# Kernel tuning notes

Measured on AMD Instinct MI355X. Metric: run time of the kernel, lower is better.

## Reference

```python
import jax, jax.numpy as jnp
import numpy as np

N_E = 1024      # nconcepts (codebook size)
E_DIM = 64      # cdim (codebook vector dim)
BETA = 0.25
LEGACY = True


def setup_inputs() -> dict:
    key = jax.random.key(0)
    k1, k2, k3 = jax.random.split(key, 3)
    z_ = jax.random.normal(k1, (32, 256, 32, 32), jnp.float32)
    # 1x1 conv dis_modulator: 256 -> 64 channels (stored as [out, in])
    conv_w = jax.random.normal(k2, (64, 256), jnp.float32) / np.sqrt(256.0)
    conv_b = jnp.zeros((64,), jnp.float32)
    # embedding.weight.data.uniform_(-1/n_e, 1/n_e)
    emb = jax.random.uniform(k3, (N_E, E_DIM), jnp.float32, -1.0 / N_E, 1.0 / N_E)
    return {"z_": z_, "conv_w": conv_w, "conv_b": conv_b, "emb": emb}


def _forward(z_, conv_w, conv_b, emb):
    sg = jax.lax.stop_gradient
    # dis_modulator: 1x1 conv == per-pixel linear map  (B,Cin,H,W)->(B,Cout,H,W)
    z = jnp.einsum('bchw,oc->bohw', z_, conv_w) + conv_b[None, :, None, None]
    B = z.shape[0]
    # torch .view(-1, e_dim): row-major flatten of (B,C,H,W) into chunks of e_dim
    zf = z.reshape(-1, E_DIM)  # [B*C*H*W/e_dim, e_dim]

    # contrastive term: mean pairwise cosine similarity of codebook rows
    d1 = emb @ emb.T                                  # [n_e, n_e]
    norms = jnp.linalg.norm(emb, axis=1)              # [n_e]
    cosine = d1 / (norms[:, None] * norms[None, :])
    contrastive = jnp.mean(cosine)

    # squared L2 distances: ||z||^2 + ||e||^2 - 2 z.e
    d = (jnp.sum(zf * zf, axis=1, keepdims=True)
         + jnp.sum(emb * emb, axis=1)[None, :]
         - 2.0 * (zf @ emb.T))                        # [N, n_e]
    idx = jnp.argmin(d, axis=1)                       # [N]
    z_q = emb[idx].reshape(z.shape)

    if LEGACY:
        loss = jnp.mean((sg(z_q) - z) ** 2) + BETA * jnp.mean((z_q - sg(z)) ** 2)
    else:
        loss = BETA * jnp.mean((sg(z_q) - z) ** 2) + jnp.mean((z_q - sg(z)) ** 2)
    # hessian_penalty(G, z_, G_z=z): G is an affine 1x1 conv, so the central
    # second difference G(z+x) - 2G(z) + G(z-x) is identically zero -> penalty = 0.
    loss = loss + contrastive

    # straight-through estimator
    z_q_st = z + sg(z_q - z)

    # replicate source exactly: flat zeros(B*n_e) scattered at codebook indices
    sampled = jnp.zeros((B * N_E,), z.dtype).at[idx].set(1.0).reshape(B, N_E)
    min_idx = idx.reshape(B, -1)
    return z_q_st, loss, sampled, min_idx


def reference(z_, conv_w, conv_b, emb):
    z_q, loss, sampled, min_idx = _forward(z_, conv_w, conv_b, emb)
    return z_q, loss, sampled, min_idx
```

## Files before the change

### kernel.cpp

```cpp
#include <hip/hip_runtime.h>

#define BATCH   32
#define CIN     256
#define COUT    64
#define HW      1024
#define NE      1024
#define ED      64
#define NROW    32768
#define ZTOT    2097152

#define OFF_LOSS 2097152
#define OFF_SAMP 2097153
#define OFF_IDX  2129921

#define CXSTR 132
#define CWSTR 68
#define ZSTR  132
#define ESTR2 260

__global__ __launch_bounds__(256, 2) void k_pre(const float* __restrict__ x,
                                                const float* __restrict__ w,
                                                const float* __restrict__ bias,
                                                float* __restrict__ z,
                                                const float* __restrict__ emb,
                                                float* __restrict__ out_samp,
                                                float* __restrict__ enorm,
                                                float* __restrict__ cpart) {
    __shared__ float SH[64 * CXSTR + 64 * CWSTR];
    int bx = blockIdx.x;
    int t  = threadIdx.x;

    if (bx < 128) {
        out_samp[bx * 256 + t] = 0.0f;
        return;
    }
    if (bx < 144) {
        float* invl = SH;
        float* S    = SH + 64;
        int b2 = bx - 128;
        int i0 = b2 * 64;
        if (t < 64) {
            const float* e = emb + (size_t)(i0 + t) * ED;
            float r8[8];
            #pragma unroll
            for (int s = 0; s < 8; s++) { float xx = e[s]; r8[s] = xx * xx; }
            #pragma unroll
            for (int m = 1; m < 8; m++) {
                #pragma unroll
                for (int s = 0; s < 8; s++) { float xx = e[8 * m + s]; r8[s] += xx * xx; }
            }
            float en = ((r8[0] + r8[1]) + (r8[2] + r8[3])) + ((r8[4] + r8[5]) + (r8[6] + r8[7]));
            invl[t] = 1.0f / sqrtf(en);
        }
        __syncthreads();
        int d = t & 63, q = t >> 6;
        float s = 0.0f;
        #pragma unroll
        for (int m = 0; m < 16; m++) {
            int il = q + 4 * m;
            s = fmaf(emb[(size_t)(i0 + il) * ED + d], invl[il], s);
        }
        S[t] = s;
        __syncthreads();
        if (t < 64)
            cpart[b2 * 64 + t] = (S[t] + S[t + 64]) + (S[t + 128] + S[t + 192]);
        return;
    }
    if (bx < 148) {
        int j = (bx - 144) * 256 + t;
        const float* e = emb + (size_t)j * ED;
        float r8[8];
        #pragma unroll
        for (int s = 0; s < 8; s++) { float xx = e[s]; r8[s] = xx * xx; }
        #pragma unroll
        for (int m = 1; m < 8; m++) {
            #pragma unroll
            for (int s = 0; s < 8; s++) { float xx = e[8 * m + s]; r8[s] += xx * xx; }
        }
        enorm[j] = ((r8[0] + r8[1]) + (r8[2] + r8[3])) + ((r8[4] + r8[5]) + (r8[6] + r8[7]));
        return;
    }

    float* Xs = SH;
    float* Ws = SH + 64 * CXSTR;
    int cbx = bx - 148;
    int b   = cbx >> 3;
    int p0  = (cbx & 7) * 128;
    int pg  = t & 15;
    int og  = t >> 4;
    float acc[8][4];
    #pragma unroll
    for (int i = 0; i < 8; i++)
        #pragma unroll
        for (int j = 0; j < 4; j++) acc[i][j] = 0.0f;

    for (int c0 = 0; c0 < CIN; c0 += 64) {
        __syncthreads();
        {
            int u = t & 31, cc = t >> 5;
            #pragma unroll
            for (int m = 0; m < 8; m++) {
                int c = cc + 8 * m;
                float4 v = *(const float4*)&x[(size_t)(b * CIN + c0 + c) * HW + p0 + 4 * u];
                *(float4*)&Xs[c * CXSTR + 4 * u] = v;
            }
            int u2 = t & 15, o2 = t >> 4;
            #pragma unroll
            for (int m = 0; m < 4; m++) {
                int o = o2 + 16 * m;
                float4 v = *(const float4*)&w[o * CIN + c0 + 4 * u2];
                Ws[(4 * u2 + 0) * CWSTR + o] = v.x;
                Ws[(4 * u2 + 1) * CWSTR + o] = v.y;
                Ws[(4 * u2 + 2) * CWSTR + o] = v.z;
                Ws[(4 * u2 + 3) * CWSTR + o] = v.w;
            }
        }
        __syncthreads();
        #pragma unroll 4
        for (int k = 0; k < 64; k++) {
            float4 xa4 = *(const float4*)&Xs[k * CXSTR + 4 * pg];
            float4 xb4 = *(const float4*)&Xs[k * CXSTR + 64 + 4 * pg];
            float4 wv4 = *(const float4*)&Ws[k * CWSTR + 4 * og];
            float xa[8] = {xa4.x, xa4.y, xa4.z, xa4.w, xb4.x, xb4.y, xb4.z, xb4.w};
            float wb[4] = {wv4.x, wv4.y, wv4.z, wv4.w};
            #pragma unroll
            for (int i = 0; i < 8; i++)
                #pragma unroll
                for (int j = 0; j < 4; j++)
                    acc[i][j] = fmaf(xa[i], wb[j], acc[i][j]);
        }
    }
    #pragma unroll
    for (int j = 0; j < 4; j++) {
        int o = 4 * og + j;
        float bv = bias[o];
        float4 lo, hi;
        lo.x = acc[0][j] + bv; lo.y = acc[1][j] + bv;
        lo.z = acc[2][j] + bv; lo.w = acc[3][j] + bv;
        hi.x = acc[4][j] + bv; hi.y = acc[5][j] + bv;
        hi.z = acc[6][j] + bv; hi.w = acc[7][j] + bv;
        *(float4*)&z[(size_t)(b * COUT + o) * HW + p0 + 4 * pg]      = lo;
        *(float4*)&z[(size_t)(b * COUT + o) * HW + p0 + 64 + 4 * pg] = hi;
    }
}

__global__ __launch_bounds__(256, 1) void k_dist(const float* __restrict__ z,
                                                 const float* __restrict__ emb,
                                                 const float* __restrict__ enorm,
                                                 float* __restrict__ out_idx,
                                                 float* __restrict__ out_samp,
                                                 float* __restrict__ out_zq,
                                                 float* __restrict__ ssep) {
    __shared__ float zs[64 * ZSTR];
    __shared__ float es[64 * ESTR2];
    __shared__ float zn_s[128];
    __shared__ float en_s[256];
    __shared__ float warr[4];
    float* redd_s = es;
    int*   redj_s = (int*)(es + 2048);
    int*   bj_s   = (int*)(es + 4096);
    int t = threadIdx.x;
    int row0 = blockIdx.x * 128;
    int rg = t & 15;
    int cg = t >> 4;

    {
        int k = t & 63, wv = t >> 6;
        #pragma unroll
        for (int m = 0; m < 8; m++) {
            int v = wv + 4 * m;
            float4 val;
            val.x = z[(size_t)(row0 + 4 * v + 0) * ED + k];
            val.y = z[(size_t)(row0 + 4 * v + 1) * ED + k];
            val.z = z[(size_t)(row0 + 4 * v + 2) * ED + k];
            val.w = z[(size_t)(row0 + 4 * v + 3) * ED + k];
            *(float4*)&zs[k * ZSTR + 4 * v] = val;
        }
    }
    __syncthreads();
    if (t < 128) {
        float r8[8];
        #pragma unroll
        for (int s = 0; s < 8; s++) { float xx = zs[s * ZSTR + t]; r8[s] = xx * xx; }
        #pragma unroll
        for (int m = 1; m < 8; m++) {
            #pragma unroll
            for (int s = 0; s < 8; s++) { float xx = zs[(8 * m + s) * ZSTR + t]; r8[s] += xx * xx; }
        }
        zn_s[t] = ((r8[0] + r8[1]) + (r8[2] + r8[3])) + ((r8[4] + r8[5]) + (r8[6] + r8[7]));
    }

    float bestd[8];
    int   bestj[8];
    #pragma unroll
    for (int i = 0; i < 8; i++) { bestd[i] = __builtin_huge_valf(); bestj[i] = 0; }

    for (int ch = 0; ch < 4; ch++) {
        int c0 = ch * 256;
        __syncthreads();
        {
            int k = t & 63, wv = t >> 6;
            #pragma unroll
            for (int m = 0; m < 16; m++) {
                int v = wv + 4 * m;
                float4 val;
                val.x = emb[(size_t)(c0 + 4 * v + 0) * ED + k];
                val.y = emb[(size_t)(c0 + 4 * v + 1) * ED + k];
                val.z = emb[(size_t)(c0 + 4 * v + 2) * ED + k];
                val.w = emb[(size_t)(c0 + 4 * v + 3) * ED + k];
                *(float4*)&es[k * ESTR2 + 4 * v] = val;
            }
            if (t < 64) {
                float4 ev4 = *(const float4*)&enorm[c0 + 4 * t];
                *(float4*)&en_s[4 * t] = ev4;
            }
        }
        __syncthreads();

        float acc[8][16];
        #pragma unroll
        for (int i = 0; i < 8; i++)
            #pragma unroll
            for (int j = 0; j < 16; j++) acc[i][j] = 0.0f;

        #pragma unroll 2
        for (int k = 0; k < 64; k++) {
            float4 za = *(const float4*)&zs[k * ZSTR + 4 * rg];
            float4 zb = *(const float4*)&zs[k * ZSTR + 64 + 4 * rg];
            float4 e0 = *(const float4*)&es[k * ESTR2 + 16 * cg];
            float4 e1 = *(const float4*)&es[k * ESTR2 + 16 * cg + 4];
            float4 e2 = *(const float4*)&es[k * ESTR2 + 16 * cg + 8];
            float4 e3 = *(const float4*)&es[k * ESTR2 + 16 * cg + 12];
            float xa[8]  = {za.x, za.y, za.z, za.w, zb.x, zb.y, zb.z, zb.w};
            float eb[16] = {e0.x, e0.y, e0.z, e0.w, e1.x, e1.y, e1.z, e1.w,
                            e2.x, e2.y, e2.z, e2.w, e3.x, e3.y, e3.z, e3.w};
            #pragma unroll
            for (int i = 0; i < 8; i++)
                #pragma unroll
                for (int j = 0; j < 16; j++)
                    acc[i][j] = fmaf(xa[i], eb[j], acc[i][j]);
        }

        #pragma unroll
        for (int i = 0; i < 8; i++) {
            int rl = (i < 4) ? (4 * rg + i) : (64 + 4 * rg + (i - 4));
            float zn = zn_s[rl];
            #pragma unroll
            for (int j = 0; j < 16; j++) {
                int cl = 16 * cg + j;
                float A = zn + en_s[cl];
                float D = A - 2.0f * acc[i][j];
                if (D < bestd[i]) { bestd[i] = D; bestj[i] = c0 + cl; }
            }
        }
    }

    __syncthreads();
    #pragma unroll
    for (int i = 0; i < 8; i++) {
        int rl = (i < 4) ? (4 * rg + i) : (64 + 4 * rg + (i - 4));
        redd_s[cg * 128 + rl] = bestd[i];
        redj_s[cg * 128 + rl] = bestj[i];
    }
    __syncthreads();
    if (t < 128) {
        float bd = __builtin_huge_valf();
        int   bj = 0x7fffffff;
        #pragma unroll
        for (int c = 0; c < 16; c++) {
            float dd = redd_s[c * 128 + t];
            int   jj = redj_s[c * 128 + t];
            if (dd < bd || (dd == bd && jj < bj)) { bd = dd; bj = jj; }
        }
        int rowg = row0 + t;
        bj_s[t]       = bj;
        out_idx[rowg] = (float)bj;
        atomicExch(&out_samp[bj], 1.0f);
    }
    __syncthreads();

    {
        int r  = t & 127;
        int kq = t >> 7;
        int bj = bj_s[r];
        const float* er = emb + (size_t)bj * ED + kq * 32;
        float sq = 0.0f;
        #pragma unroll
        for (int m = 0; m < 8; m++) {
            float4 ev = *(const float4*)&er[4 * m];
            int kk = kq * 32 + 4 * m;
            float zv0 = zs[(kk + 0) * ZSTR + r];
            float zv1 = zs[(kk + 1) * ZSTR + r];
            float zv2 = zs[(kk + 2) * ZSTR + r];
            float zv3 = zs[(kk + 3) * ZSTR + r];
            float d0 = ev.x - zv0, d1 = ev.y - zv1, d2 = ev.z - zv2, d3 = ev.w - zv3;
            float4 o4;
            o4.x = zv0 + d0; o4.y = zv1 + d1; o4.z = zv2 + d2; o4.w = zv3 + d3;
            *(float4*)&out_zq[(size_t)(row0 + r) * ED + kk] = o4;
            sq += d0 * d0; sq += d1 * d1; sq += d2 * d2; sq += d3 * d3;
        }
        #pragma unroll
        for (int off = 32; off > 0; off >>= 1) sq += __shfl_down(sq, off, 64);
        if ((t & 63) == 0) warr[t >> 6] = sq;
    }
    __syncthreads();
    if (t == 0)
        ssep[blockIdx.x] = (warr[0] + warr[1]) + (warr[2] + warr[3]);
}

__global__ __launch_bounds__(256) void k_final(const float* __restrict__ ssep,
                                               const float* __restrict__ cpart,
                                               float* __restrict__ out_loss) {
    __shared__ double SD[256];
    __shared__ float  CS;
    int t = threadIdx.x;
    SD[t] = (double)ssep[t];
    __syncthreads();
    #pragma unroll
    for (int off = 128; off > 0; off >>= 1) {
        if (t < off) SD[t] += SD[t + off];
        __syncthreads();
    }
    if (t < 64) {
        float v = 0.0f;
        #pragma unroll
        for (int m = 0; m < 16; m++) v += cpart[m * 64 + t];
        float sq = v * v;
        #pragma unroll
        for (int off = 32; off > 0; off >>= 1) sq += __shfl_down(sq, off, 64);
        if (t == 0) CS = sq / (1024.0f * 1024.0f);
    }
    __syncthreads();
    if (t == 0) {
        float m = (float)(SD[0] / (double)ZTOT);
        float loss = m + 0.25f * m;
        out_loss[0] = loss + CS;
    }
}

extern "C" void kernel_launch(void* const* d_in, const int* in_sizes, int n_in,
                              void* d_out, int out_size, void* d_ws, size_t ws_size,
                              hipStream_t stream) {
    (void)in_sizes; (void)n_in; (void)out_size; (void)ws_size;
    const float* z_     = (const float*)d_in[0];
    const float* conv_w = (const float*)d_in[1];
    const float* conv_b = (const float*)d_in[2];
    const float* emb    = (const float*)d_in[3];

    float* out      = (float*)d_out;
    float* out_zq   = out;
    float* out_loss = out + OFF_LOSS;
    float* out_samp = out + OFF_SAMP;
    float* out_idx  = out + OFF_IDX;

    char*  ws       = (char*)d_ws;
    float* wz       = (float*)ws;
    float* enorm    = (float*)(ws + 8388608);
    float* cpart    = (float*)(ws + 8396800);
    float* ssep     = (float*)(ws + 8400896);

    k_pre  <<<404, 256, 0, stream>>>(z_, conv_w, conv_b, wz, emb, out_samp, enorm, cpart);
    k_dist <<<256, 256, 0, stream>>>(wz, emb, enorm, out_idx, out_samp, out_zq, ssep);
    k_final<<<1,   256, 0, stream>>>(ssep, cpart, out_loss);
}
```

Baseline: 179.5 us.

## Shrink distance tile to raise occupancy and fold final reduction into last block

```diff
diff --git a/kernel.cpp b/kernel.cpp
--- a/kernel.cpp
+++ b/kernel.cpp
@@ -16,7 +16,7 @@
 #define CXSTR 132
 #define CWSTR 68
 #define ZSTR  132
-#define ESTR2 260
+#define ESTR  132
 
 __global__ __launch_bounds__(256, 2) void k_pre(const float* __restrict__ x,
                                                 const float* __restrict__ w,
@@ -25,12 +25,14 @@
                                                 const float* __restrict__ emb,
                                                 float* __restrict__ out_samp,
                                                 float* __restrict__ enorm,
-                                                float* __restrict__ cpart) {
+                                                float* __restrict__ cpart,
+                                                unsigned int* __restrict__ counter) {
     __shared__ float SH[64 * CXSTR + 64 * CWSTR];
     int bx = blockIdx.x;
     int t  = threadIdx.x;
 
     if (bx < 128) {
+        if (bx == 0 && t == 0) *counter = 0u;
         out_samp[bx * 256 + t] = 0.0f;
         return;
     }
@@ -144,18 +146,23 @@
     }
 }
 
-__global__ __launch_bounds__(256, 1) void k_dist(const float* __restrict__ z,
+__global__ __launch_bounds__(256, 2) void k_dist(const float* __restrict__ z,
                                                  const float* __restrict__ emb,
                                                  const float* __restrict__ enorm,
+                                                 const float* __restrict__ cpart,
                                                  float* __restrict__ out_idx,
                                                  float* __restrict__ out_samp,
                                                  float* __restrict__ out_zq,
-                                                 float* __restrict__ ssep) {
+                                                 float* __restrict__ ssep,
+                                                 float* __restrict__ out_loss,
+                                                 unsigned int* __restrict__ counter) {
     __shared__ float zs[64 * ZSTR];
-    __shared__ float es[64 * ESTR2];
+    __shared__ float es[64 * ESTR];
     __shared__ float zn_s[128];
-    __shared__ float en_s[256];
+    __shared__ float en_s[128];
     __shared__ float warr[4];
+    __shared__ int   lastflag;
+    __shared__ float CS;
     float* redd_s = es;
     int*   redj_s = (int*)(es + 2048);
     int*   bj_s   = (int*)(es + 4096);
@@ -195,49 +202,46 @@
     #pragma unroll
     for (int i = 0; i < 8; i++) { bestd[i] = __builtin_huge_valf(); bestj[i] = 0; }
 
-    for (int ch = 0; ch < 4; ch++) {
-        int c0 = ch * 256;
+    for (int ch = 0; ch < 8; ch++) {
+        int c0 = ch * 128;
         __syncthreads();
         {
             int k = t & 63, wv = t >> 6;
             #pragma unroll
-            for (int m = 0; m < 16; m++) {
+            for (int m = 0; m < 8; m++) {
                 int v = wv + 4 * m;
                 float4 val;
                 val.x = emb[(size_t)(c0 + 4 * v + 0) * ED + k];
                 val.y = emb[(size_t)(c0 + 4 * v + 1) * ED + k];
                 val.z = emb[(size_t)(c0 + 4 * v + 2) * ED + k];
                 val.w = emb[(size_t)(c0 + 4 * v + 3) * ED + k];
-                *(float4*)&es[k * ESTR2 + 4 * v] = val;
-            }
-            if (t < 64) {
+                *(float4*)&es[k * ESTR + 4 * v] = val;
+            }
+            if (t < 32) {
                 float4 ev4 = *(const float4*)&enorm[c0 + 4 * t];
                 *(float4*)&en_s[4 * t] = ev4;
             }
         }
         __syncthreads();
 
-        float acc[8][16];
+        float acc[8][8];
         #pragma unroll
         for (int i = 0; i < 8; i++)
             #pragma unroll
-            for (int j = 0; j < 16; j++) acc[i][j] = 0.0f;
-
-        #pragma unroll 2
+            for (int j = 0; j < 8; j++) acc[i][j] = 0.0f;
+
+        #pragma unroll 4
         for (int k = 0; k < 64; k++) {
             float4 za = *(const float4*)&zs[k * ZSTR + 4 * rg];
             float4 zb = *(const float4*)&zs[k * ZSTR + 64 + 4 * rg];
-            float4 e0 = *(const float4*)&es[k * ESTR2 + 16 * cg];
-            float4 e1 = *(const float4*)&es[k * ESTR2 + 16 * cg + 4];
-            float4 e2 = *(const float4*)&es[k * ESTR2 + 16 * cg + 8];
-            float4 e3 = *(const float4*)&es[k * ESTR2 + 16 * cg + 12];
-            float xa[8]  = {za.x, za.y, za.z, za.w, zb.x, zb.y, zb.z, zb.w};
-            float eb[16] = {e0.x, e0.y, e0.z, e0.w, e1.x, e1.y, e1.z, e1.w,
-                            e2.x, e2.y, e2.z, e2.w, e3.x, e3.y, e3.z, e3.w};
+            float4 e0 = *(const float4*)&es[k * ESTR + 8 * cg];
+            float4 e1 = *(const float4*)&es[k * ESTR + 8 * cg + 4];
+            float xa[8] = {za.x, za.y, za.z, za.w, zb.x, zb.y, zb.z, zb.w};
+            float eb[8] = {e0.x, e0.y, e0.z, e0.w, e1.x, e1.y, e1.z, e1.w};
             #pragma unroll
             for (int i = 0; i < 8; i++)
                 #pragma unroll
-                for (int j = 0; j < 16; j++)
+                for (int j = 0; j < 8; j++)
                     acc[i][j] = fmaf(xa[i], eb[j], acc[i][j]);
         }
 
@@ -246,8 +250,8 @@
             int rl = (i < 4) ? (4 * rg + i) : (64 + 4 * rg + (i - 4));
             float zn = zn_s[rl];
             #pragma unroll
-            for (int j = 0; j < 16; j++) {
-                int cl = 16 * cg + j;
+            for (int j = 0; j < 8; j++) {
+                int cl = 8 * cg + j;
                 float A = zn + en_s[cl];
                 float D = A - 2.0f * acc[i][j];
                 if (D < bestd[i]) { bestd[i] = D; bestj[i] = c0 + cl; }
@@ -304,37 +308,40 @@
         if ((t & 63) == 0) warr[t >> 6] = sq;
     }
     __syncthreads();
-    if (t == 0)
+
+    if (t == 0) {
         ssep[blockIdx.x] = (warr[0] + warr[1]) + (warr[2] + warr[3]);
-}
-
-__global__ __launch_bounds__(256) void k_final(const float* __restrict__ ssep,
-                                               const float* __restrict__ cpart,
-                                               float* __restrict__ out_loss) {
-    __shared__ double SD[256];
-    __shared__ float  CS;
-    int t = threadIdx.x;
-    SD[t] = (double)ssep[t];
-    __syncthreads();
-    #pragma unroll
-    for (int off = 128; off > 0; off >>= 1) {
-        if (t < off) SD[t] += SD[t + off];
-        __syncthreads();
-    }
-    if (t < 64) {
-        float v = 0.0f;
-        #pragma unroll
-        for (int m = 0; m < 16; m++) v += cpart[m * 64 + t];
-        float sq = v * v;
-        #pragma unroll
-        for (int off = 32; off > 0; off >>= 1) sq += __shfl_down(sq, off, 64);
-        if (t == 0) CS = sq / (1024.0f * 1024.0f);
-    }
-    __syncthreads();
-    if (t == 0) {
-        float m = (float)(SD[0] / (double)ZTOT);
-        float loss = m + 0.25f * m;
-        out_loss[0] = loss + CS;
+        __threadfence();
+        unsigned int old = atomicAdd(counter, 1u);
+        lastflag = (old == 255u) ? 1 : 0;
+    }
+    __syncthreads();
+    if (lastflag) {
+        __threadfence();
+        double* SD = (double*)es;
+        const volatile float* sv = (const volatile float*)ssep;
+        SD[t] = (double)sv[t];
+        __syncthreads();
+        #pragma unroll
+        for (int off = 128; off > 0; off >>= 1) {
+            if (t < off) SD[t] += SD[t + off];
+            __syncthreads();
+        }
+        if (t < 64) {
+            float v = 0.0f;
+            #pragma unroll
+            for (int m = 0; m < 16; m++) v += cpart[m * 64 + t];
+            float sq = v * v;
+            #pragma unroll
+            for (int off = 32; off > 0; off >>= 1) sq += __shfl_down(sq, off, 64);
+            if (t == 0) CS = sq / (1024.0f * 1024.0f);
+        }
+        __syncthreads();
+        if (t == 0) {
+            float m = (float)(SD[0] / (double)ZTOT);
+            float loss = m + 0.25f * m;
+            out_loss[0] = loss + CS;
+        }
     }
 }
 
@@ -356,10 +363,10 @@
     char*  ws       = (char*)d_ws;
     float* wz       = (float*)ws;
     float* enorm    = (float*)(ws + 8388608);
-    float* cpart    = (float*)(ws + 8396800);
-    float* ssep     = (float*)(ws + 8400896);
-
-    k_pre  <<<404, 256, 0, stream>>>(z_, conv_w, conv_b, wz, emb, out_samp, enorm, cpart);
-    k_dist <<<256, 256, 0, stream>>>(wz, emb, enorm, out_idx, out_samp, out_zq, ssep);
-    k_final<<<1,   256, 0, stream>>>(ssep, cpart, out_loss);
+    float* cpart    = (float*)(ws + 8392704);
+    float* ssep     = (float*)(ws + 8396800);
+    unsigned int* counter = (unsigned int*)(ws + 8397824);
+
+    k_pre  <<<404, 256, 0, stream>>>(z_, conv_w, conv_b, wz, emb, out_samp, enorm, cpart, counter);
+    k_dist <<<256, 256, 0, stream>>>(wz, emb, enorm, cpart, out_idx, out_samp, out_zq, ssep, out_loss, counter);
 }
```

After: 183.9 us. 2.4% more time.
